# Kernel optimization log

Measured on AMD Instinct MI355X. Metric: run time of the kernel, lower is better.

Reference implementation:

```python
import jax, jax.numpy as jnp
import numpy as np

N = 100000
F_IN = 128
DIM = 2
E = 3200000


def setup_inputs() -> dict:
    key = jax.random.key(0)
    k1, k2, k3, k4, k5, k6, k7 = jax.random.split(key, 7)
    x = jax.random.normal(k1, (N, F_IN), dtype=jnp.float32)
    edge_index = jax.random.randint(k2, (2, E), 0, N, dtype=jnp.int64)
    edge_attr = jax.random.uniform(k3, (E,), dtype=jnp.float32)
    # GCNConv params: lin weight [F_IN, DIM] (glorot), bias zeros
    conv_w = jax.random.normal(k4, (F_IN, DIM), dtype=jnp.float32) * (1.0 / np.sqrt(F_IN))
    conv_b = jnp.zeros((DIM,), dtype=jnp.float32)
    # TopKPooling score weight [DIM]
    pool_w = jax.random.normal(k5, (DIM,), dtype=jnp.float32)
    # fc: Linear(N*DIM, 1), init normal(0, 0.01), bias 0 (per init_weights)
    fc_w = jax.random.normal(k6, (N * DIM, 1), dtype=jnp.float32) * 0.01
    fc_b = jnp.zeros((1,), dtype=jnp.float32)
    return {"x": x, "edge_index": edge_index, "edge_attr": edge_attr,
            "conv_w": conv_w, "conv_b": conv_b, "pool_w": pool_w,
            "fc_w": fc_w, "fc_b": fc_b}


def reference(x, edge_index, edge_attr, conv_w, conv_b, pool_w, fc_w, fc_b):
    n = x.shape[0]
    row, col = edge_index[0], edge_index[1]
    # --- GCNConv: add self-loops (weight 1), symmetric normalization ---
    loop = jnp.arange(n, dtype=edge_index.dtype)
    row_f = jnp.concatenate([row, loop])
    col_f = jnp.concatenate([col, loop])
    w_f = jnp.concatenate([edge_attr, jnp.ones((n,), dtype=x.dtype)])
    deg = jax.ops.segment_sum(w_f, col_f, num_segments=n)  # [N]
    dinv = jnp.where(deg > 0, jax.lax.rsqrt(deg), 0.0)
    norm = dinv[row_f] * w_f * dinv[col_f]  # [E+N]
    h = x @ conv_w  # [N, DIM] transform-then-propagate
    msg = norm[:, None] * h[row_f]  # [E+N, DIM]
    out = jax.ops.segment_sum(msg, col_f, num_segments=n) + conv_b  # [N, DIM]
    # --- ReLU ---
    out = jax.nn.relu(out)
    # --- TopKPooling with k = N (single graph): score, sort desc, gate ---
    score = jnp.tanh((out @ pool_w) / jnp.linalg.norm(pool_w))  # [N]
    perm = jnp.argsort(-score)
    pooled = out[perm] * score[perm][:, None]  # [N, DIM]
    # --- flatten + fc + sigmoid ---
    flat = pooled.reshape(-1)  # [N*DIM]
    y = jax.nn.sigmoid(flat @ fc_w + fc_b)  # [1]
    return y
```

## Files before the change

### kernel.cpp

```cpp
#include <hip/hip_runtime.h>
#include <math.h>

#define FIN 128
#define W 512
#define S 16
#define MAXG 256
#define CAP 18432u
#define HB 256
#define HT 1024
#define BP 200

__device__ __forceinline__ long long edge_at(const void* p, long long i, unsigned mode) {
  return mode ? ((const long long*)p)[i] : (long long)((const int*)p)[i];
}

__device__ __forceinline__ void atomic_fadd(float* p, float v) {
  __hip_atomic_fetch_add(p, v, __ATOMIC_RELAXED, __HIP_MEMORY_SCOPE_AGENT);
}

__device__ __forceinline__ void lds_fadd(float* p, float v) {
  unsafeAtomicAdd(p, v);
}

__global__ void k_detect(const unsigned* ei, unsigned* mode, float* acc,
                         unsigned* cur, int G, unsigned* ticket) {
  int t = threadIdx.x;
  if (t == 0) {
    unsigned orv = 0;
    for (int i = 1; i < 1024; i += 2) orv |= ei[i];
    *mode = (orv == 0) ? 1u : 0u;
    *acc = 0.0f;
    *ticket = 0u;
  }
  for (int i = t; i < G; i += 64) cur[i] = (unsigned)i * CAP;
}

__global__ void k_h(const float* __restrict__ x, const float* __restrict__ cw,
                    float* __restrict__ h, int n) {
  int gt = blockIdx.x * blockDim.x + threadIdx.x;
  int node = gt >> 5;
  int sub = gt & 31;
  if (node >= n) return;
  float4 xv = ((const float4*)x)[node * 32 + sub];
  float s0 = xv.x * cw[sub * 8 + 0] + xv.y * cw[sub * 8 + 2] +
             xv.z * cw[sub * 8 + 4] + xv.w * cw[sub * 8 + 6];
  float s1 = xv.x * cw[sub * 8 + 1] + xv.y * cw[sub * 8 + 3] +
             xv.z * cw[sub * 8 + 5] + xv.w * cw[sub * 8 + 7];
  for (int off = 16; off > 0; off >>= 1) {
    s0 += __shfl_down(s0, off, 32);
    s1 += __shfl_down(s1, off, 32);
  }
  if (sub == 0) { h[node * 2] = s0; h[node * 2 + 1] = s1; }
}

__global__ void k_scatter2(const void* ei, const float* __restrict__ attr,
                           long long E, int G, unsigned* cur,
                           uint2* __restrict__ packed,
                           const unsigned* __restrict__ mode) {
  __shared__ unsigned hist[MAXG];
  __shared__ unsigned base[MAXG];
  unsigned m = *mode;
  int t = threadIdx.x;
  if (t < MAXG) hist[t] = 0;
  __syncthreads();
  long long perB = (E + HB - 1) / HB;
  long long b0 = (long long)blockIdx.x * perB;
  long long lim = b0 + perB; if (lim > E) lim = E;
  long long e = b0 + t;
  for (; e + 3LL * HT < lim; e += 4LL * HT) {
    int c0 = (int)edge_at(ei, E + e, m);
    int c1 = (int)edge_at(ei, E + e + HT, m);
    int c2 = (int)edge_at(ei, E + e + 2 * HT, m);
    int c3 = (int)edge_at(ei, E + e + 3 * HT, m);
    atomicAdd(&hist[c0 >> 9], 1u);
    atomicAdd(&hist[c1 >> 9], 1u);
    atomicAdd(&hist[c2 >> 9], 1u);
    atomicAdd(&hist[c3 >> 9], 1u);
  }
  for (; e < lim; e += HT) {
    int c = (int)edge_at(ei, E + e, m);
    atomicAdd(&hist[c >> 9], 1u);
  }
  __syncthreads();
  if (t < G) base[t] = atomicAdd(&cur[t], hist[t]);
  __syncthreads();
  e = b0 + t;
  for (; e + 3LL * HT < lim; e += 4LL * HT) {
    int r0 = (int)edge_at(ei, e, m),          c0 = (int)edge_at(ei, E + e, m);
    int r1 = (int)edge_at(ei, e + HT, m),     c1 = (int)edge_at(ei, E + e + HT, m);
    int r2 = (int)edge_at(ei, e + 2 * HT, m), c2 = (int)edge_at(ei, E + e + 2 * HT, m);
    int r3 = (int)edge_at(ei, e + 3 * HT, m), c3 = (int)edge_at(ei, E + e + 3 * HT, m);
    float a0 = attr[e], a1 = attr[e + HT], a2 = attr[e + 2 * HT], a3 = attr[e + 3 * HT];
    unsigned p0 = atomicAdd(&base[c0 >> 9], 1u);
    packed[p0] = make_uint2(((unsigned)r0 << 9) | ((unsigned)c0 & 511u), __float_as_uint(a0));
    unsigned p1 = atomicAdd(&base[c1 >> 9], 1u);
    packed[p1] = make_uint2(((unsigned)r1 << 9) | ((unsigned)c1 & 511u), __float_as_uint(a1));
    unsigned p2 = atomicAdd(&base[c2 >> 9], 1u);
    packed[p2] = make_uint2(((unsigned)r2 << 9) | ((unsigned)c2 & 511u), __float_as_uint(a2));
    unsigned p3 = atomicAdd(&base[c3 >> 9], 1u);
    packed[p3] = make_uint2(((unsigned)r3 << 9) | ((unsigned)c3 & 511u), __float_as_uint(a3));
  }
  for (; e < lim; e += HT) {
    int r = (int)edge_at(ei, e, m);
    int c = (int)edge_at(ei, E + e, m);
    float a = attr[e];
    unsigned pos = atomicAdd(&base[c >> 9], 1u);
    packed[pos] = make_uint2(((unsigned)r << 9) | ((unsigned)c & 511u), __float_as_uint(a));
  }
}

__global__ void k_deginv(const uint2* __restrict__ packed, const unsigned* __restrict__ cur,
                         const float* __restrict__ h, float* __restrict__ dinv,
                         float* __restrict__ gv, int n) {
  __shared__ float sdeg[W];
  int g = blockIdx.x, t = threadIdx.x;
  sdeg[t] = 0.f;
  __syncthreads();
  unsigned lo = (unsigned)g * CAP, hi = cur[g];
  for (unsigned b = lo + t; b < hi; b += 4 * 512) {
    unsigned k1 = b + 512, k2 = b + 1024, k3 = b + 1536;
    uint2 p0 = packed[b];
    uint2 p1 = packed[k1 < hi ? k1 : b];
    uint2 p2 = packed[k2 < hi ? k2 : b];
    uint2 p3 = packed[k3 < hi ? k3 : b];
    lds_fadd(&sdeg[p0.x & (W - 1u)], __uint_as_float(p0.y));
    if (k1 < hi) lds_fadd(&sdeg[p1.x & (W - 1u)], __uint_as_float(p1.y));
    if (k2 < hi) lds_fadd(&sdeg[p2.x & (W - 1u)], __uint_as_float(p2.y));
    if (k3 < hi) lds_fadd(&sdeg[p3.x & (W - 1u)], __uint_as_float(p3.y));
  }
  __syncthreads();
  int c = g * W + t;
  if (c < n) {
    float di = rsqrtf(1.0f + sdeg[t]);
    dinv[c] = di;
    gv[2 * c]     = di * h[2 * c];
    gv[2 * c + 1] = di * h[2 * c + 1];
  }
}

__global__ void k_pmsg(const uint2* __restrict__ packed, const unsigned* __restrict__ cur,
                       const float* __restrict__ gv, float* __restrict__ pacc) {
  __shared__ float sacc[2 * W];
  int blk = blockIdx.x, t = threadIdx.x;
  int g = blk >> 4, s = blk & (S - 1);
#pragma unroll
  for (int i = 0; i < 4; ++i) sacc[t + 256 * i] = 0.f;
  __syncthreads();
  unsigned lo = (unsigned)g * CAP, hi = cur[g];
  unsigned len = hi - lo;
  unsigned per = (len + S - 1) / S;
  unsigned mylo = lo + s * per;
  unsigned myhi = mylo + per; if (myhi > hi) myhi = hi;
  const float2* g2 = (const float2*)gv;
  for (unsigned b = mylo + t; b < myhi; b += 4 * 256) {
    unsigned k1 = b + 256, k2 = b + 512, k3 = b + 768;
    uint2 p0 = packed[b];
    uint2 p1 = packed[k1 < myhi ? k1 : b];
    uint2 p2 = packed[k2 < myhi ? k2 : b];
    uint2 p3 = packed[k3 < myhi ? k3 : b];
    float2 g0 = g2[p0.x >> 9];
    float2 g1 = g2[p1.x >> 9];
    float2 g2v = g2[p2.x >> 9];
    float2 g3 = g2[p3.x >> 9];
    float a0 = __uint_as_float(p0.y), a1 = __uint_as_float(p1.y);
    float a2 = __uint_as_float(p2.y), a3 = __uint_as_float(p3.y);
    unsigned c0 = p0.x & (W - 1u), c1 = p1.x & (W - 1u);
    unsigned c2 = p2.x & (W - 1u), c3 = p3.x & (W - 1u);
    lds_fadd(&sacc[2 * c0],     a0 * g0.x);
    lds_fadd(&sacc[2 * c0 + 1], a0 * g0.y);
    if (k1 < myhi) { lds_fadd(&sacc[2 * c1], a1 * g1.x); lds_fadd(&sacc[2 * c1 + 1], a1 * g1.y); }
    if (k2 < myhi) { lds_fadd(&sacc[2 * c2], a2 * g2v.x); lds_fadd(&sacc[2 * c2 + 1], a2 * g2v.y); }
    if (k3 < myhi) { lds_fadd(&sacc[2 * c3], a3 * g3.x); lds_fadd(&sacc[2 * c3 + 1], a3 * g3.y); }
  }
  __syncthreads();
#pragma unroll
  for (int i = 0; i < 4; ++i) pacc[(size_t)blk * (2 * W) + t + 256 * i] = sacc[t + 256 * i];
}

__global__ void k_gout(const float* __restrict__ pacc, const float* __restrict__ dinv,
                       const float* __restrict__ h, const float* __restrict__ cb,
                       const float* __restrict__ pw, float* __restrict__ out,
                       float* __restrict__ score, unsigned* __restrict__ keys,
                       unsigned* __restrict__ table, int n) {
  __shared__ unsigned hist[256];
  int g = blockIdx.x, t = threadIdx.x;
  if (t < 256) hist[t] = 0;
  __syncthreads();
  const float2* p2 = (const float2*)pacc;
  float a0 = 0.f, a1 = 0.f;
#pragma unroll
  for (int s = 0; s < S; ++s) {
    float2 v = p2[(size_t)(g * S + s) * W + t];
    a0 += v.x; a1 += v.y;
  }
  int c = g * W + t;
  if (c < n) {
    float dc = dinv[c];
    float o0 = fmaxf(dc * a0 + dc * dc * h[2 * c]     + cb[0], 0.f);
    float o1 = fmaxf(dc * a1 + dc * dc * h[2 * c + 1] + cb[1], 0.f);
    out[2 * c] = o0; out[2 * c + 1] = o1;
    float pw0 = pw[0], pw1 = pw[1];
    float s = tanhf((o0 * pw0 + o1 * pw1) / sqrtf(pw0 * pw0 + pw1 * pw1));
    score[c] = s;
    unsigned u = __float_as_uint(s);
    unsigned asc = u ^ ((u >> 31) ? 0xFFFFFFFFu : 0x80000000u);
    unsigned key = ~asc;
    keys[c] = key;
    atomicAdd(&hist[key & 255u], 1u);
  }
  __syncthreads();
  if (t < 256) table[t * BP + g] = hist[t];
}

__global__ void k_rhist(const unsigned* __restrict__ keys, int n, int shift,
                        unsigned* table) {
  __shared__ unsigned hist[256];
  int t = threadIdx.x;
  if (t < 256) hist[t] = 0;
  __syncthreads();
  int g = blockIdx.x * 512 + t;
  if (g < n) atomicAdd(&hist[(keys[g] >> shift) & 255u], 1u);
  __syncthreads();
  if (t < 256) table[t * BP + blockIdx.x] = hist[t];
}

__global__ void k_rscat(const unsigned* __restrict__ keysIn,
                        const unsigned* __restrict__ payIn, int n, int shift,
                        const unsigned* __restrict__ table,
                        unsigned* keysOut, unsigned* payOut, int flags) {
  __shared__ unsigned pfx[256];
  __shared__ unsigned scn[256];
  __shared__ unsigned waveCnt[8 * 256];
  int b = blockIdx.x, t = threadIdx.x;
  int lane = t & 63, w = t >> 6;
  int nblk = gridDim.x;
  unsigned rt_total = 0;
  if (t < 256) {
    const unsigned* row = table + t * BP;
    unsigned partial = 0, total = 0;
#pragma unroll 4
    for (int i = 0; i < nblk; ++i) {
      unsigned v = row[i];
      total += v;
      partial += (i < b) ? v : 0u;
    }
    rt_total = total;
    scn[t] = total;
    pfx[t] = partial;
  }
  __syncthreads();
  for (int off = 1; off < 256; off <<= 1) {
    unsigned add = 0;
    if (t < 256 && t >= off) add = scn[t - off];
    __syncthreads();
    if (t < 256) scn[t] += add;
    __syncthreads();
  }
  if (t < 256) pfx[t] += scn[t] - rt_total;
  for (int q = t; q < 8 * 256; q += 512) waveCnt[q] = 0;
  __syncthreads();
  int g = b * 512 + t;
  bool active = g < n;
  unsigned key = 0, pay = 0, d = 0;
  if (active) {
    key = keysIn[g];
    pay = (flags & 1) ? (unsigned)g : payIn[g];
    d = (key >> shift) & 255u;
  }
  unsigned long long am = __ballot(active);
  unsigned long long mm = ~0ull;
#pragma unroll
  for (int bb = 0; bb < 8; ++bb) {
    unsigned long long bl = __ballot((d >> bb) & 1u);
    mm &= ((d >> bb) & 1u) ? bl : ~bl;
  }
  mm &= am;
  int rankw = __popcll(mm & ((1ull << lane) - 1ull));
  if (active && rankw == 0) waveCnt[w * 256 + d] = (unsigned)__popcll(mm);
  __syncthreads();
  if (active) {
    unsigned o = (unsigned)rankw;
    for (int ww = 0; ww < w; ++ww) o += waveCnt[ww * 256 + d];
    unsigned gpos = pfx[d] + o;
    if (!(flags & 2)) keysOut[gpos] = key;
    payOut[gpos] = pay;
  }
}

__global__ void k_final(const unsigned* __restrict__ perm, const float* __restrict__ out,
                        const float* __restrict__ score, const float* __restrict__ fcw,
                        const float* __restrict__ fcb, float* acc, unsigned* ticket,
                        float* y, int n) {
  __shared__ float red[4];
  int stride = gridDim.x * blockDim.x;
  float s = 0.f;
  const float2* o2 = (const float2*)out;
  const float2* f2 = (const float2*)fcw;
  for (int j = blockIdx.x * blockDim.x + threadIdx.x; j < n; j += stride) {
    unsigned p = perm[j];
    float2 ov = o2[p];
    float2 fv = f2[j];
    s += score[p] * (ov.x * fv.x + ov.y * fv.y);
  }
  int lane = threadIdx.x & 63, w = threadIdx.x >> 6;
  for (int off = 32; off > 0; off >>= 1) s += __shfl_down(s, off);
  if (lane == 0) red[w] = s;
  __syncthreads();
  if (threadIdx.x == 0) {
    float bs = red[0] + red[1] + red[2] + red[3];
    atomic_fadd(acc, bs);
    __threadfence();
    unsigned old = __hip_atomic_fetch_add(ticket, 1u, __ATOMIC_ACQ_REL,
                                          __HIP_MEMORY_SCOPE_AGENT);
    if (old == (unsigned)(gridDim.x - 1)) {
      float z = __hip_atomic_fetch_add(acc, 0.0f, __ATOMIC_ACQUIRE,
                                       __HIP_MEMORY_SCOPE_AGENT);
      y[0] = 1.f / (1.f + expf(-(z + fcb[0])));
    }
  }
}

extern "C" void kernel_launch(void* const* d_in, const int* in_sizes, int n_in,
                              void* d_out, int out_size, void* d_ws, size_t ws_size,
                              hipStream_t stream) {
  const float* x     = (const float*)d_in[0];
  const void*  ei    = d_in[1];
  const float* attr  = (const float*)d_in[2];
  const float* convw = (const float*)d_in[3];
  const float* convb = (const float*)d_in[4];
  const float* poolw = (const float*)d_in[5];
  const float* fcw   = (const float*)d_in[6];
  const float* fcb   = (const float*)d_in[7];
  float* y = (float*)d_out;

  int N = in_sizes[0] / FIN;
  long long E = in_sizes[2];
  int G = (N + W - 1) / W;

  float* ws = (float*)d_ws;
  size_t off = 0;
  uint2* packed  = (uint2*)(ws + off); off += (size_t)2 * G * CAP;
  float* pacc    = ws + off; off += (size_t)2 * G * S * W;
  float* h       = ws + off; off += (size_t)2 * N;
  float* dinv    = ws + off; off += (size_t)N;
  float* gv      = ws + off; off += (size_t)2 * N;
  float* outN    = ws + off; off += (size_t)2 * N;
  float* score   = ws + off; off += (size_t)N;
  unsigned* keysA = (unsigned*)(ws + off); off += (size_t)N;
  unsigned* payA  = (unsigned*)(ws + off); off += (size_t)N;
  unsigned* keysB = (unsigned*)(ws + off); off += (size_t)N;
  unsigned* payB  = (unsigned*)(ws + off); off += (size_t)N;
  unsigned* cur   = (unsigned*)(ws + off); off += (size_t)G;
  unsigned* stab  = (unsigned*)(ws + off); off += (size_t)256 * BP;
  float* acc      = ws + off; off += 1;
  unsigned* mode  = (unsigned*)(ws + off); off += 1;
  unsigned* ticket = (unsigned*)(ws + off); off += 1;

  k_detect<<<1, 64, 0, stream>>>((const unsigned*)ei, mode, acc, cur, G, ticket);
  k_h<<<(N * 32 + 255) / 256, 256, 0, stream>>>(x, convw, h, N);

  k_scatter2<<<HB, HT, 0, stream>>>(ei, attr, E, G, cur, packed, mode);

  k_deginv<<<G, W, 0, stream>>>(packed, cur, h, dinv, gv, N);
  k_pmsg<<<G * S, 256, 0, stream>>>(packed, cur, gv, pacc);
  k_gout<<<G, W, 0, stream>>>(pacc, dinv, h, convb, poolw, outN, score, keysA, stab, N);

  k_rscat<<<G, 512, 0, stream>>>(keysA, payB, N, 0, stab, keysB, payB, 1);
  k_rhist<<<G, 512, 0, stream>>>(keysB, N, 8, stab);
  k_rscat<<<G, 512, 0, stream>>>(keysB, payB, N, 8, stab, keysA, payA, 0);
  k_rhist<<<G, 512, 0, stream>>>(keysA, N, 16, stab);
  k_rscat<<<G, 512, 0, stream>>>(keysA, payA, N, 16, stab, keysB, payB, 0);
  k_rhist<<<G, 512, 0, stream>>>(keysB, N, 24, stab);
  k_rscat<<<G, 512, 0, stream>>>(keysB, payB, N, 24, stab, keysA, payA, 2);

  k_final<<<G, 256, 0, stream>>>(payA, outN, score, fcw, fcb, acc, ticket, y, N);
}
```

Baseline: 199.5 us.

## Stage edge bucketing in LDS and write packed edges in contiguous runs

```diff
diff --git a/kernel.cpp b/kernel.cpp
--- a/kernel.cpp
+++ b/kernel.cpp
@@ -6,13 +6,9 @@
 #define S 16
 #define MAXG 256
 #define CAP 18432u
-#define HB 256
-#define HT 1024
+#define TILE 12544
+#define HTS 1024
 #define BP 200
-
-__device__ __forceinline__ long long edge_at(const void* p, long long i, unsigned mode) {
-  return mode ? ((const long long*)p)[i] : (long long)((const int*)p)[i];
-}
 
 __device__ __forceinline__ void atomic_fadd(float* p, float v) {
   __hip_atomic_fetch_add(p, v, __ATOMIC_RELAXED, __HIP_MEMORY_SCOPE_AGENT);
@@ -53,59 +49,61 @@
   if (sub == 0) { h[node * 2] = s0; h[node * 2 + 1] = s1; }
 }
 
-__global__ void k_scatter2(const void* ei, const float* __restrict__ attr,
+__global__ void k_scatter3(const void* ei, const float* __restrict__ attr,
                            long long E, int G, unsigned* cur,
                            uint2* __restrict__ packed,
                            const unsigned* __restrict__ mode) {
+  __shared__ uint2 stage[TILE];
+  __shared__ unsigned char gid[TILE];
   __shared__ unsigned hist[MAXG];
-  __shared__ unsigned base[MAXG];
+  __shared__ unsigned lofs[MAXG];
+  __shared__ unsigned wofs[MAXG];
+  __shared__ unsigned gbase[MAXG];
   unsigned m = *mode;
   int t = threadIdx.x;
-  if (t < MAXG) hist[t] = 0;
-  __syncthreads();
-  long long perB = (E + HB - 1) / HB;
+  long long perB = (E + gridDim.x - 1) / gridDim.x;
   long long b0 = (long long)blockIdx.x * perB;
   long long lim = b0 + perB; if (lim > E) lim = E;
-  long long e = b0 + t;
-  for (; e + 3LL * HT < lim; e += 4LL * HT) {
-    int c0 = (int)edge_at(ei, E + e, m);
-    int c1 = (int)edge_at(ei, E + e + HT, m);
-    int c2 = (int)edge_at(ei, E + e + 2 * HT, m);
-    int c3 = (int)edge_at(ei, E + e + 3 * HT, m);
-    atomicAdd(&hist[c0 >> 9], 1u);
-    atomicAdd(&hist[c1 >> 9], 1u);
-    atomicAdd(&hist[c2 >> 9], 1u);
-    atomicAdd(&hist[c3 >> 9], 1u);
-  }
-  for (; e < lim; e += HT) {
-    int c = (int)edge_at(ei, E + e, m);
+  int nE = (int)(lim > b0 ? lim - b0 : 0);
+  if (t < MAXG) hist[t] = 0;
+  __syncthreads();
+  for (int i = t; i < nE; i += HTS) {
+    long long e = b0 + i;
+    int c = m ? (int)((const long long*)ei)[E + e] : ((const int*)ei)[E + e];
     atomicAdd(&hist[c >> 9], 1u);
   }
   __syncthreads();
-  if (t < G) base[t] = atomicAdd(&cur[t], hist[t]);
-  __syncthreads();
-  e = b0 + t;
-  for (; e + 3LL * HT < lim; e += 4LL * HT) {
-    int r0 = (int)edge_at(ei, e, m),          c0 = (int)edge_at(ei, E + e, m);
-    int r1 = (int)edge_at(ei, e + HT, m),     c1 = (int)edge_at(ei, E + e + HT, m);
-    int r2 = (int)edge_at(ei, e + 2 * HT, m), c2 = (int)edge_at(ei, E + e + 2 * HT, m);
-    int r3 = (int)edge_at(ei, e + 3 * HT, m), c3 = (int)edge_at(ei, E + e + 3 * HT, m);
-    float a0 = attr[e], a1 = attr[e + HT], a2 = attr[e + 2 * HT], a3 = attr[e + 3 * HT];
-    unsigned p0 = atomicAdd(&base[c0 >> 9], 1u);
-    packed[p0] = make_uint2(((unsigned)r0 << 9) | ((unsigned)c0 & 511u), __float_as_uint(a0));
-    unsigned p1 = atomicAdd(&base[c1 >> 9], 1u);
-    packed[p1] = make_uint2(((unsigned)r1 << 9) | ((unsigned)c1 & 511u), __float_as_uint(a1));
-    unsigned p2 = atomicAdd(&base[c2 >> 9], 1u);
-    packed[p2] = make_uint2(((unsigned)r2 << 9) | ((unsigned)c2 & 511u), __float_as_uint(a2));
-    unsigned p3 = atomicAdd(&base[c3 >> 9], 1u);
-    packed[p3] = make_uint2(((unsigned)r3 << 9) | ((unsigned)c3 & 511u), __float_as_uint(a3));
-  }
-  for (; e < lim; e += HT) {
-    int r = (int)edge_at(ei, e, m);
-    int c = (int)edge_at(ei, E + e, m);
+  if (t < MAXG) lofs[t] = hist[t];
+  __syncthreads();
+  for (int off = 1; off < MAXG; off <<= 1) {
+    unsigned add = 0;
+    if (t < MAXG && t >= off) add = lofs[t - off];
+    __syncthreads();
+    if (t < MAXG) lofs[t] += add;
+    __syncthreads();
+  }
+  if (t < MAXG) {
+    unsigned excl = lofs[t] - hist[t];
+    lofs[t] = excl;
+    wofs[t] = excl;
+    gbase[t] = (t < G && hist[t] != 0u) ? atomicAdd(&cur[t], hist[t]) : 0u;
+  }
+  __syncthreads();
+  for (int i = t; i < nE; i += HTS) {
+    long long e = b0 + i;
+    int r, c;
+    if (m) { r = (int)((const long long*)ei)[e]; c = (int)((const long long*)ei)[E + e]; }
+    else   { r = ((const int*)ei)[e];            c = ((const int*)ei)[E + e]; }
     float a = attr[e];
-    unsigned pos = atomicAdd(&base[c >> 9], 1u);
-    packed[pos] = make_uint2(((unsigned)r << 9) | ((unsigned)c & 511u), __float_as_uint(a));
+    int g = c >> 9;
+    unsigned pos = atomicAdd(&wofs[g], 1u);
+    stage[pos] = make_uint2(((unsigned)r << 9) | ((unsigned)c & 511u), __float_as_uint(a));
+    gid[pos] = (unsigned char)g;
+  }
+  __syncthreads();
+  for (int i = t; i < nE; i += HTS) {
+    unsigned g = gid[i];
+    packed[gbase[g] + (unsigned)i - lofs[g]] = stage[i];
   }
 }
 
@@ -336,6 +334,8 @@
   int N = in_sizes[0] / FIN;
   long long E = in_sizes[2];
   int G = (N + W - 1) / W;
+  int HBn = (int)((E + TILE - 1) / TILE);
+  if (HBn < 256) HBn = 256;
 
   float* ws = (float*)d_ws;
   size_t off = 0;
@@ -359,7 +359,7 @@
   k_detect<<<1, 64, 0, stream>>>((const unsigned*)ei, mode, acc, cur, G, ticket);
   k_h<<<(N * 32 + 255) / 256, 256, 0, stream>>>(x, convw, h, N);
 
-  k_scatter2<<<HB, HT, 0, stream>>>(ei, attr, E, G, cur, packed, mode);
+  k_scatter3<<<HBn, HTS, 0, stream>>>(ei, attr, E, G, cur, packed, mode);
 
   k_deginv<<<G, W, 0, stream>>>(packed, cur, h, dinv, gv, N);
   k_pmsg<<<G * S, 256, 0, stream>>>(packed, cur, gv, pacc);
```

After: 201.1 us. No clear change (+0.8%).
